# Kernel tuning notes

Measured on AMD Instinct MI355X. Metric: run time of the kernel, lower is better.

Reference implementation:

```python
import jax, jax.numpy as jnp
import numpy as np
import math

S, B, E, H = 2048, 2, 1024, 16
HD = E // H
NEG_INF = -jnp.inf


def setup_inputs() -> dict:
    key = jax.random.key(0)
    ks = jax.random.split(key, 6)
    query = jax.random.normal(ks[0], (S, B, E), dtype=jnp.float32)
    relative_pos_bias = jax.random.normal(ks[1], (H, S, S), dtype=jnp.float32)
    # causal float mask: 0 where allowed, -inf where disallowed (code tests attn_mask == -inf)
    causal = jnp.tril(jnp.ones((S, S), dtype=bool))
    attn_mask = jnp.where(causal, 0.0, NEG_INF).astype(jnp.float32)
    key_padding_mask = jnp.zeros((B, S), dtype=bool)
    in_proj_weight = jax.random.normal(ks[2], (3 * E, E), dtype=jnp.float32) / math.sqrt(E)
    in_proj_bias = jax.random.normal(ks[3], (3 * E,), dtype=jnp.float32) * 0.01
    out_proj_weight = jax.random.normal(ks[4], (E, E), dtype=jnp.float32) / math.sqrt(E)
    out_proj_bias = jax.random.normal(ks[5], (E,), dtype=jnp.float32) * 0.01
    return {
        "query": query,
        "relative_pos_bias": relative_pos_bias,
        "attn_mask": attn_mask,
        "key_padding_mask": key_padding_mask,
        "in_proj_weight": in_proj_weight,
        "in_proj_bias": in_proj_bias,
        "out_proj_weight": out_proj_weight,
        "out_proj_bias": out_proj_bias,
    }


def _nan_to_zero(x):
    return jnp.where(jnp.isnan(x), jnp.zeros_like(x), x)


def reference(query, relative_pos_bias, attn_mask, key_padding_mask,
              in_proj_weight, in_proj_bias, out_proj_weight, out_proj_bias):
    s, b, e = query.shape
    h, hd = H, HD
    # fused QKV projection from query (self-attention, matches F.linear(q, in_proj_weight))
    qkv = query @ in_proj_weight.T + in_proj_bias          # (S, B, 3E)
    q, k, v = jnp.split(qkv, 3, axis=-1)                   # each (S, B, E)
    # (S, B, E) -> (B, H, S, hd); torch does view(S, B*H, hd).transpose(0,1)
    def to_heads(x):
        return x.reshape(s, b, h, hd).transpose(1, 2, 0, 3)  # (B, H, S, hd)
    q, k, v = to_heads(q), to_heads(k), to_heads(v)
    scores = jnp.einsum("bhsd,bhtd->bhst", q, k) / math.sqrt(hd)  # (B, H, S, S)
    bias = jnp.clip(relative_pos_bias, -5.0, 5.0)
    scores = scores + bias[None] * 0.05
    scores = jnp.clip(scores, -30.0, 30.0)
    # attn_mask: -inf entries get masked
    scores = jnp.where((attn_mask == NEG_INF)[None, None], NEG_INF, scores)
    # key padding mask: True -> masked
    scores = jnp.where(key_padding_mask[:, None, None, :], NEG_INF, scores)
    attn_weights = jax.nn.softmax(scores, axis=-1)         # stable (max-subtracted)
    out = jnp.einsum("bhst,bhtd->bshd", attn_weights, v)   # (B, S, H, hd)
    out = _nan_to_zero(out).reshape(b, s, e)
    out = jnp.clip(out, -10.0, 10.0)
    out = out @ out_proj_weight.T + out_proj_bias
    out = _nan_to_zero(out)
    return out.transpose(1, 0, 2)                          # (S, B, E), batch_first=False
```

## Files before the change

### kernel.cpp

```cpp
#include <hip/hip_runtime.h>
#include <cstdint>

#define SS 2048
#define BB 2
#define EE 1024
#define HH 16
#define DD 64

typedef _Float16 f16;
typedef __attribute__((ext_vector_type(8))) _Float16 f16x8;
typedef __attribute__((ext_vector_type(4))) _Float16 f16x4;
typedef __attribute__((ext_vector_type(4))) float f32x4;

__device__ __forceinline__ f32x4 mfma16(f16x8 a, f16x8 b, f32x4 c) {
  return __builtin_amdgcn_mfma_f32_16x16x32_f16(a, b, c, 0, 0, 0);
}

__device__ __forceinline__ void gload16(void* lds, const void* g) {
  __builtin_amdgcn_global_load_lds((const __attribute__((address_space(1))) void*)g,
                                   (__attribute__((address_space(3))) void*)lds, 16, 0, 0);
}

__global__ void k_convert(const float* __restrict__ x, const float* __restrict__ wi,
                          const float* __restrict__ wo,
                          f16* __restrict__ xb, f16* __restrict__ wib, f16* __restrict__ wob) {
  const int N0 = 1048576, N1 = 786432, N2 = 262144;
  const int total = N0 + N1 + N2;
  for (int i = blockIdx.x * blockDim.x + threadIdx.x; i < total; i += gridDim.x * blockDim.x) {
    const float4* src; f16* dst; int off;
    if (i < N0)            { src = (const float4*)x;  dst = xb;  off = i; }
    else if (i < N0 + N1)  { src = (const float4*)wi; dst = wib; off = i - N0; }
    else                   { src = (const float4*)wo; dst = wob; off = i - N0 - N1; }
    float4 v = src[off];
    f16x4 o;
    o[0] = (f16)v.x; o[1] = (f16)v.y; o[2] = (f16)v.z; o[3] = (f16)v.w;
    *(f16x4*)(dst + (int64_t)off * 4) = o;
  }
}

template <int MODE>
__global__ __launch_bounds__(256) void k_gemm(
    const f16* __restrict__ A, const f16* __restrict__ Bw, const float* __restrict__ bias,
    f16* __restrict__ qo, f16* __restrict__ ko, f16* __restrict__ vo, float* __restrict__ fo) {
  __shared__ __align__(16) f16 As[128 * 32];
  __shared__ __align__(16) f16 Bs[128 * 32];
  const int tid = threadIdx.x;
  const int w = tid >> 6, lane = tid & 63, g = lane >> 4, l4 = lane & 15;
  const int bm = blockIdx.y * 128, bn = blockIdx.x * 128;
  const int wr = (w >> 1) * 64, wc = (w & 1) * 64;
  f32x4 acc[4][4] = {};

  const f16* asrc[2]; const f16* bsrc[2]; f16* adst[2]; f16* bdst[2];
#pragma unroll
  for (int r = 0; r < 2; ++r) {
    int c = r * 256 + tid, row = c >> 2, cc = c & 3;
    asrc[r] = A + (int64_t)(bm + row) * 1024 + cc * 8;
    bsrc[r] = Bw + (int64_t)(bn + row) * 1024 + cc * 8;
    adst[r] = As + (r * 256 + w * 64) * 8;
    bdst[r] = Bs + (r * 256 + w * 64) * 8;
  }

  for (int kt = 0; kt < 1024; kt += 32) {
#pragma unroll
    for (int r = 0; r < 2; ++r) {
      gload16(adst[r], asrc[r] + kt);
      gload16(bdst[r], bsrc[r] + kt);
    }
    __syncthreads();
    f16x8 af[4], bf[4];
#pragma unroll
    for (int i = 0; i < 4; ++i) af[i] = *(const f16x8*)(As + (wr + i * 16 + l4) * 32 + g * 8);
#pragma unroll
    for (int j = 0; j < 4; ++j) bf[j] = *(const f16x8*)(Bs + (wc + j * 16 + l4) * 32 + g * 8);
#pragma unroll
    for (int i = 0; i < 4; ++i)
#pragma unroll
      for (int j = 0; j < 4; ++j)
        acc[i][j] = mfma16(af[i], bf[j], acc[i][j]);
    __syncthreads();
  }

#pragma unroll
  for (int i = 0; i < 4; ++i) {
#pragma unroll
    for (int j = 0; j < 4; ++j) {
      int n = bn + wc + j * 16 + l4;
      float bv = bias[n];
#pragma unroll
      for (int r = 0; r < 4; ++r) {
        int m = bm + wr + i * 16 + g * 4 + r;
        float v = acc[i][j][r] + bv;
        if (MODE == 1) {
          fo[(int64_t)m * EE + n] = v;
        } else {
          int part = n >> 10, e = n & 1023, hh = e >> 6, d = e & 63;
          int s = m >> 1, b = m & 1;
          int64_t idx = (((int64_t)(b * HH + hh)) * SS + s) * DD + d;
          if (part == 0)      qo[idx] = (f16)(v * 0.125f);
          else if (part == 1) ko[idx] = (f16)v;
          else                vo[idx] = (f16)v;
        }
      }
    }
  }
}

__global__ __launch_bounds__(256) void k_vtrans(const f16* __restrict__ vin, f16* __restrict__ vt) {
  __shared__ f16 t[64 * 65];
  const int bh = blockIdx.y;
  const int s0 = blockIdx.x * 64;
  const int tid = threadIdx.x;
#pragma unroll
  for (int r = 0; r < 2; ++r) {
    int c = r * 256 + tid, row = c >> 3, cc = c & 7;
    f16x8 v = *(const f16x8*)(vin + ((int64_t)bh * SS + s0 + row) * DD + cc * 8);
#pragma unroll
    for (int j = 0; j < 8; ++j) t[row * 65 + cc * 8 + j] = v[j];
  }
  __syncthreads();
#pragma unroll
  for (int r = 0; r < 2; ++r) {
    int c = r * 256 + tid, d = c >> 3, cc = c & 7;
    f16x8 o;
#pragma unroll
    for (int j = 0; j < 8; ++j) o[j] = t[(cc * 8 + j) * 65 + d];
    *(f16x8*)(vt + ((int64_t)bh * DD + d) * SS + s0 + cc * 8) = o;
  }
}

__global__ __launch_bounds__(256) void k_attn(
    const f16* __restrict__ Qg, const f16* __restrict__ Kg, const f16* __restrict__ Vtg,
    const float* __restrict__ rpb, f16* __restrict__ Og) {
  __shared__ __align__(16) f16 Kt[2][64 * 64];
  __shared__ __align__(16) f16 Vt[2][64 * 64];
  __shared__ __align__(16) f16 Pt[64 * 64];
  __shared__ float sc_lds[64];
  __shared__ float li_lds[64];
  const int b = blockIdx.x, p = blockIdx.y, h = blockIdx.z;
  const int tid = threadIdx.x, w = tid >> 6, lane = tid & 63, g = lane >> 4, l4 = lane & 15;
  const int bh = b * HH + h;
  const float* rpbb = rpb + (int64_t)h * SS * SS;

#define ATTN_ITER(KT_, BCUR, BNXT)                                                      \
  {                                                                                     \
    const int kt_ = (KT_);                                                              \
    const int cur_ = kt_ & 1;                                                           \
    const int ks_ = kt_ * 64;                                                           \
    const bool pf_ = (kt_ < qt);                                                        \
    if (pf_) {                                                                          \
      const int ksn_ = ks_ + 64;                                                        \
      _Pragma("unroll")                                                                 \
      for (int r_ = 0; r_ < 2; ++r_) {                                                  \
        const int c_ = r_ * 256 + tid, row_ = c_ >> 3, cc_ = c_ & 7;                    \
        const int sc_ = cc_ ^ (row_ & 7);                                               \
        gload16(&Kt[cur_ ^ 1][(r_ * 256 + w * 64) * 8],                                 \
                Kg + ((int64_t)bh * SS + ksn_ + row_) * DD + sc_ * 8);                  \
        gload16(&Vt[cur_ ^ 1][(r_ * 256 + w * 64) * 8],                                 \
                Vtg + ((int64_t)bh * DD + row_) * SS + ksn_ + sc_ * 8);                 \
      }                                                                                 \
      asm volatile("" ::: "memory");           \
      _Pragma("unroll")                                                                 \
      for (int rg_ = 0; rg_ < 4; ++rg_)                                                 \
        _Pragma("unroll")                                                               \
        for (int j_ = 0; j_ < 4; ++j_)                                                  \
          BNXT[rg_ * 4 + j_] =                                                          \
              rpbb[(int64_t)(qrow + g * 4 + rg_) * SS + ksn_ + j_ * 16 + l4];           \
    }                                                                                   \
    f32x4 sf_[4] = {};                                                                  \
    _Pragma("unroll")                                                                   \
    for (int ki_ = 0; ki_ < 2; ++ki_)                                                   \
      _Pragma("unroll")                                                                 \
      for (int j_ = 0; j_ < 4; ++j_) {                                                  \
        const int row_ = j_ * 16 + l4;                                                  \
        const int ch_ = (ki_ * 4 + g) ^ (row_ & 7);                                     \
        f16x8 bk_ = *(const f16x8*)(&Kt[cur_][row_ * 64 + ch_ * 8]);                    \
        sf_[j_] = mfma16(qf[ki_], bk_, sf_[j_]);                                        \
      }                                                                                 \
    _Pragma("unroll")                                                                   \
    for (int rg_ = 0; rg_ < 4; ++rg_) {                                                 \
      const int qg_ = qrow + g * 4 + rg_;                                               \
      float pv_[4]; float mx_ = -INFINITY;                                              \
      _Pragma("unroll")                                                                 \
      for (int j_ = 0; j_ < 4; ++j_) {                                                  \
        const int kc_ = ks_ + j_ * 16 + l4;                                             \
        float bs_ = fminf(fmaxf(BCUR[rg_ * 4 + j_], -5.f), 5.f);                        \
        float v_ = sf_[j_][rg_] + 0.05f * bs_;                                          \
        v_ = fminf(fmaxf(v_, -30.f), 30.f);                                             \
        v_ = (kc_ > qg_) ? -INFINITY : v_;                                              \
        pv_[j_] = v_; mx_ = fmaxf(mx_, v_);                                             \
      }                                                                                 \
      _Pragma("unroll")                                                                 \
      for (int d_ = 1; d_ < 16; d_ <<= 1) mx_ = fmaxf(mx_, __shfl_xor(mx_, d_));        \
      const float mnew_ = fmaxf(m_run[rg_], mx_);                                       \
      const float scl_ = exp2f((m_run[rg_] - mnew_) * 1.44269504f);                     \
      float rsum_ = 0.f;                                                                \
      _Pragma("unroll")                                                                 \
      for (int j_ = 0; j_ < 4; ++j_) {                                                  \
        const float e_ = exp2f((pv_[j_] - mnew_) * 1.44269504f);                        \
        pv_[j_] = e_; rsum_ += e_;                                                      \
      }                                                                                 \
      _Pragma("unroll")                                                                 \
      for (int d_ = 1; d_ < 16; d_ <<= 1) rsum_ += __shfl_xor(rsum_, d_);               \
      l_run[rg_] = l_run[rg_] * scl_ + rsum_;                                           \
      m_run[rg_] = mnew_;                                                               \
      const int prow_ = w * 16 + g * 4 + rg_;                                           \
      if (l4 == 0) sc_lds[prow_] = scl_;                                                \
      _Pragma("unroll")                                                                 \
      for (int j_ = 0; j_ < 4; ++j_) {                                                  \
        const int col_ = j_ * 16 + l4;                                                  \
        const int ch_ = (col_ >> 3) ^ (prow_ & 7);                                      \
        Pt[prow_ * 64 + ch_ * 8 + (col_ & 7)] = (f16)pv_[j_];                           \
      }                                                                                 \
    }                                                                                   \
                                \
    const float osc_ = sc_lds[w * 16 + l4];                                             \
    _Pragma("unroll")                                                                   \
    for (int dt_ = 0; dt_ < 4; ++dt_) {                                                 \
      oacc[dt_][0] *= osc_; oacc[dt_][1] *= osc_;                                       \
      oacc[dt_][2] *= osc_; oacc[dt_][3] *= osc_;                                       \
    }                                                                                   \
    _Pragma("unroll")                                                                   \
    for (int ki_ = 0; ki_ < 2; ++ki_) {                                                 \
      const int prow_ = w * 16 + l4;                                                    \
      const int pch_ = (ki_ * 4 + g) ^ (prow_ & 7);                                     \
      f16x8 pb_ = *(const f16x8*)(&Pt[prow_ * 64 + pch_ * 8]);                          \
      _Pragma("unroll")                                                                 \
      for (int dt_ = 0; dt_ < 4; ++dt_) {                                               \
        const int vrow_ = dt_ * 16 + l4;                                                \
        const int vch_ = (ki_ * 4 + g) ^ (vrow_ & 7);                                   \
        f16x8 av_ = *(const f16x8*)(&Vt[cur_][vrow_ * 64 + vch_ * 8]);                  \
        oacc[dt_] = mfma16(av_, pb_, oacc[dt_]);                                        \
      }                                                                                 \
    }                                                                                   \
    asm volatile("s_waitcnt vmcnt(16)" ::: "memory");     \
    __builtin_amdgcn_s_barrier();                                                       \
  }

  for (int half = 0; half < 2; ++half) {
    const int qt = half ? p : (31 - p);
    const int qs = qt * 64;
    const int qrow = qs + w * 16;

    f16x8 qf[2];
    {
      const f16* qb = Qg + ((int64_t)bh * SS + qrow + l4) * DD + g * 8;
      qf[0] = *(const f16x8*)qb;
      qf[1] = *(const f16x8*)(qb + 32);
    }

    float bA[16], bB[16];
#pragma unroll
    for (int r_ = 0; r_ < 2; ++r_) {
      const int c_ = r_ * 256 + tid, row_ = c_ >> 3, cc_ = c_ & 7;
      const int sc_ = cc_ ^ (row_ & 7);
      gload16(&Kt[0][(r_ * 256 + w * 64) * 8], Kg + ((int64_t)bh * SS + row_) * DD + sc_ * 8);
      gload16(&Vt[0][(r_ * 256 + w * 64) * 8], Vtg + ((int64_t)bh * DD + row_) * SS + sc_ * 8);
    }
    asm volatile("" ::: "memory");
#pragma unroll
    for (int rg_ = 0; rg_ < 4; ++rg_)
#pragma unroll
      for (int j_ = 0; j_ < 4; ++j_)
        bA[rg_ * 4 + j_] = rpbb[(int64_t)(qrow + g * 4 + rg_) * SS + j_ * 16 + l4];
    asm volatile("s_waitcnt vmcnt(16)" ::: "memory");
    __builtin_amdgcn_s_barrier();

    f32x4 oacc[4] = {};
    float m_run[4], l_run[4];
#pragma unroll
    for (int r = 0; r < 4; ++r) { m_run[r] = -INFINITY; l_run[r] = 0.f; }

    int kt = 0;
    while (kt + 2 <= qt + 1) {
      ATTN_ITER(kt, bA, bB)
      ATTN_ITER(kt + 1, bB, bA)
      kt += 2;
    }
    if (kt <= qt) ATTN_ITER(kt, bA, bB)

    if (l4 == 0) {
#pragma unroll
      for (int rg = 0; rg < 4; ++rg) li_lds[w * 16 + g * 4 + rg] = 1.f / l_run[rg];
    }
    const float linv = li_lds[w * 16 + l4];
#pragma unroll
    for (int dt = 0; dt < 4; ++dt) {
#pragma unroll
      for (int r = 0; r < 4; ++r) {
        int d = dt * 16 + g * 4 + r;
        int ql = w * 16 + l4;
        float o = oacc[dt][r] * linv;
        o = fminf(fmaxf(o, -10.f), 10.f);
        int ch = (d >> 3) ^ (ql & 7);
        Pt[ql * 64 + ch * 8 + (d & 7)] = (f16)o;
      }
    }
    __syncthreads();
#pragma unroll
    for (int r = 0; r < 2; ++r) {
      int c = r * 256 + tid, row = c >> 3, cc = c & 7;
      int sc = cc ^ (row & 7);
      f16x8 ov = *(const f16x8*)(&Pt[row * 64 + sc * 8]);
      *(f16x8*)(Og + (((int64_t)(qs + row)) * BB + b) * EE + h * DD + cc * 8) = ov;
    }
  }
#undef ATTN_ITER
}

extern "C" void kernel_launch(void* const* d_in, const int* in_sizes, int n_in,
                              void* d_out, int out_size, void* d_ws, size_t ws_size,
                              hipStream_t stream) {
  (void)in_sizes; (void)n_in; (void)out_size; (void)ws_size;
  const float* query = (const float*)d_in[0];
  const float* rpb   = (const float*)d_in[1];
  const float* w_in  = (const float*)d_in[4];
  const float* b_in  = (const float*)d_in[5];
  const float* w_out = (const float*)d_in[6];
  const float* b_out = (const float*)d_in[7];
  float* out = (float*)d_out;

  f16* Xb  = (f16*)d_ws;
  f16* Wib = Xb + 4194304;
  f16* Wob = Wib + 3145728;
  f16* Qb  = Wob + 1048576;
  f16* Kb  = Qb + 4194304;
  f16* Vb  = Kb + 4194304;
  f16* Vtb = Vb + 4194304;
  f16* Ob  = Xb;

  k_convert<<<2048, 256, 0, stream>>>(query, w_in, w_out, Xb, Wib, Wob);
  k_gemm<0><<<dim3(24, 32), 256, 0, stream>>>(Xb, Wib, b_in, Qb, Kb, Vb, nullptr);
  k_vtrans<<<dim3(32, 32), 256, 0, stream>>>(Vb, Vtb);
  k_attn<<<dim3(2, 16, 16), 256, 0, stream>>>(Qb, Kb, Vtb, rpb, Ob);
  k_gemm<1><<<dim3(8, 32), 256, 0, stream>>>(Ob, Wob, b_out, nullptr, nullptr, nullptr, out);
}
```

Measured before the change: 496.0 us.

## Fuse V transpose into QKV GEMM epilogue and retile output projection

The QKV GEMM epilogue now stages its tile in shared memory. It writes Q/K as vectorized 16-byte stores and writes V directly in transposed layout, so the separate transpose kernel and the intermediate V buffer go away. The output projection GEMM uses 64-row tiles, which doubles its grid from 256 to 512 blocks and gives better occupancy on the many-CU device. The cost is a large extra LDS allocation (about 34KB) in the QKV kernel, plus strided LDS reads for the transposed V writes.

```diff
diff --git a/kernel.cpp b/kernel.cpp
--- a/kernel.cpp
+++ b/kernel.cpp
@@ -38,12 +38,12 @@
   }
 }
 
-template <int MODE>
-__global__ __launch_bounds__(256) void k_gemm(
+__global__ __launch_bounds__(256) void k_gemm_qkv(
     const f16* __restrict__ A, const f16* __restrict__ Bw, const float* __restrict__ bias,
-    f16* __restrict__ qo, f16* __restrict__ ko, f16* __restrict__ vo, float* __restrict__ fo) {
+    f16* __restrict__ qo, f16* __restrict__ ko, f16* __restrict__ vt) {
   __shared__ __align__(16) f16 As[128 * 32];
   __shared__ __align__(16) f16 Bs[128 * 32];
+  __shared__ __align__(16) f16 Cs[128 * 136];
   const int tid = threadIdx.x;
   const int w = tid >> 6, lane = tid & 63, g = lane >> 4, l4 = lane & 15;
   const int bm = blockIdx.y * 128, bn = blockIdx.x * 128;
@@ -80,52 +80,98 @@
     __syncthreads();
   }
 
-#pragma unroll
-  for (int i = 0; i < 4; ++i) {
+  const int part = bn >> 10;
+  const int baseh = (bn & 1023) >> 6;
+  const float scale = (part == 0) ? 0.125f : 1.0f;
+
+#pragma unroll
+  for (int j = 0; j < 4; ++j) {
+    const float bv = bias[bn + wc + j * 16 + l4];
+#pragma unroll
+    for (int i = 0; i < 4; ++i)
+#pragma unroll
+      for (int r = 0; r < 4; ++r)
+        Cs[(wr + i * 16 + g * 4 + r) * 136 + wc + j * 16 + l4] =
+            (f16)((acc[i][j][r] + bv) * scale);
+  }
+  __syncthreads();
+
+  if (part < 2) {
+    f16* dst = (part == 0) ? qo : ko;
+#pragma unroll
+    for (int it = 0; it < 8; ++it) {
+      const int item = it * 256 + tid;
+      const int m = item >> 4, c = item & 15;
+      const int hh = baseh + (c >> 3), d0 = (c & 7) * 8;
+      f16x8 v = *(const f16x8*)(Cs + m * 136 + (c >> 3) * 64 + d0);
+      const int s = (bm >> 1) + (m >> 1), bq = m & 1;
+      *(f16x8*)(dst + (((int64_t)(bq * HH + hh)) * SS + s) * DD + d0) = v;
+    }
+  } else {
+#pragma unroll
+    for (int it = 0; it < 8; ++it) {
+      const int item = it * 256 + tid;
+      const int s0 = item & 7, bq = (item >> 3) & 1, col = item >> 4;
+      const int hh = baseh + (col >> 6), d = col & 63;
+      f16x8 v;
+#pragma unroll
+      for (int k = 0; k < 8; ++k) v[k] = Cs[((s0 * 8 + k) * 2 + bq) * 136 + col];
+      *(f16x8*)(vt + (((int64_t)(bq * HH + hh)) * DD + d) * SS + (bm >> 1) + s0 * 8) = v;
+    }
+  }
+}
+
+__global__ __launch_bounds__(256) void k_gemm_out(
+    const f16* __restrict__ A, const f16* __restrict__ Bw, const float* __restrict__ bias,
+    float* __restrict__ fo) {
+  __shared__ __align__(16) f16 As[64 * 32];
+  __shared__ __align__(16) f16 Bs[128 * 32];
+  const int tid = threadIdx.x;
+  const int w = tid >> 6, lane = tid & 63, g = lane >> 4, l4 = lane & 15;
+  const int bm = blockIdx.y * 64, bn = blockIdx.x * 128;
+  const int wr = (w >> 1) * 32, wc = (w & 1) * 64;
+  f32x4 acc[2][4] = {};
+
+  const f16* asrc = A + (int64_t)(bm + (tid >> 2)) * 1024 + (tid & 3) * 8;
+  f16* adst = As + (w * 64) * 8;
+  const f16* bsrc[2]; f16* bdst[2];
+#pragma unroll
+  for (int r = 0; r < 2; ++r) {
+    int c = r * 256 + tid, row = c >> 2, cc = c & 3;
+    bsrc[r] = Bw + (int64_t)(bn + row) * 1024 + cc * 8;
+    bdst[r] = Bs + (r * 256 + w * 64) * 8;
+  }
+
+  for (int kt = 0; kt < 1024; kt += 32) {
+    gload16(adst, asrc + kt);
+#pragma unroll
+    for (int r = 0; r < 2; ++r) gload16(bdst[r], bsrc[r] + kt);
+    __syncthreads();
+    f16x8 af[2], bf[4];
+#pragma unroll
+    for (int i = 0; i < 2; ++i) af[i] = *(const f16x8*)(As + (wr + i * 16 + l4) * 32 + g * 8);
+#pragma unroll
+    for (int j = 0; j < 4; ++j) bf[j] = *(const f16x8*)(Bs + (wc + j * 16 + l4) * 32 + g * 8);
+#pragma unroll
+    for (int i = 0; i < 2; ++i)
+#pragma unroll
+      for (int j = 0; j < 4; ++j)
+        acc[i][j] = mfma16(af[i], bf[j], acc[i][j]);
+    __syncthreads();
+  }
+
+#pragma unroll
+  for (int i = 0; i < 2; ++i)
 #pragma unroll
     for (int j = 0; j < 4; ++j) {
-      int n = bn + wc + j * 16 + l4;
-      float bv = bias[n];
+      const int n = bn + wc + j * 16 + l4;
+      const float bv = bias[n];
 #pragma unroll
       for (int r = 0; r < 4; ++r) {
-        int m = bm + wr + i * 16 + g * 4 + r;
-        float v = acc[i][j][r] + bv;
-        if (MODE == 1) {
-          fo[(int64_t)m * EE + n] = v;
-        } else {
-          int part = n >> 10, e = n & 1023, hh = e >> 6, d = e & 63;
-          int s = m >> 1, b = m & 1;
-          int64_t idx = (((int64_t)(b * HH + hh)) * SS + s) * DD + d;
-          if (part == 0)      qo[idx] = (f16)(v * 0.125f);
-          else if (part == 1) ko[idx] = (f16)v;
-          else                vo[idx] = (f16)v;
-        }
+        const int m = bm + wr + i * 16 + g * 4 + r;
+        fo[(int64_t)m * EE + n] = acc[i][j][r] + bv;
       }
     }
-  }
-}
-
-__global__ __launch_bounds__(256) void k_vtrans(const f16* __restrict__ vin, f16* __restrict__ vt) {
-  __shared__ f16 t[64 * 65];
-  const int bh = blockIdx.y;
-  const int s0 = blockIdx.x * 64;
-  const int tid = threadIdx.x;
-#pragma unroll
-  for (int r = 0; r < 2; ++r) {
-    int c = r * 256 + tid, row = c >> 3, cc = c & 7;
-    f16x8 v = *(const f16x8*)(vin + ((int64_t)bh * SS + s0 + row) * DD + cc * 8);
-#pragma unroll
-    for (int j = 0; j < 8; ++j) t[row * 65 + cc * 8 + j] = v[j];
-  }
-  __syncthreads();
-#pragma unroll
-  for (int r = 0; r < 2; ++r) {
-    int c = r * 256 + tid, d = c >> 3, cc = c & 7;
-    f16x8 o;
-#pragma unroll
-    for (int j = 0; j < 8; ++j) o[j] = t[(cc * 8 + j) * 65 + d];
-    *(f16x8*)(vt + ((int64_t)bh * DD + d) * SS + s0 + cc * 8) = o;
-  }
 }
 
 __global__ __launch_bounds__(256) void k_attn(
@@ -324,13 +370,11 @@
   f16* Wob = Wib + 3145728;
   f16* Qb  = Wob + 1048576;
   f16* Kb  = Qb + 4194304;
-  f16* Vb  = Kb + 4194304;
-  f16* Vtb = Vb + 4194304;
+  f16* Vtb = Kb + 4194304;
   f16* Ob  = Xb;
 
   k_convert<<<2048, 256, 0, stream>>>(query, w_in, w_out, Xb, Wib, Wob);
-  k_gemm<0><<<dim3(24, 32), 256, 0, stream>>>(Xb, Wib, b_in, Qb, Kb, Vb, nullptr);
-  k_vtrans<<<dim3(32, 32), 256, 0, stream>>>(Vb, Vtb);
+  k_gemm_qkv<<<dim3(24, 32), 256, 0, stream>>>(Xb, Wib, b_in, Qb, Kb, Vtb);
   k_attn<<<dim3(2, 16, 16), 256, 0, stream>>>(Qb, Kb, Vtb, rpb, Ob);
-  k_gemm<1><<<dim3(8, 32), 256, 0, stream>>>(Ob, Wob, b_out, nullptr, nullptr, nullptr, out);
-}
+  k_gemm_out<<<dim3(8, 64), 256, 0, stream>>>(Ob, Wob, b_out, out);
+}
```

After: 493.1 us. No clear change (-0.6%).
